# Kernel optimization log

Hardware: AMD Instinct MI355X
Metric: run time of the kernel (lower is better)

The kernel has to match this reference:

```python
import jax, jax.numpy as jnp
import numpy as np

B, S, D, H, E, K, F = 2, 512, 768, 12, 8, 2, 3072
HD = D // H
EPS = 1e-5


def setup_inputs() -> dict:
    key = jax.random.key(0)
    ks = jax.random.split(key, 8)
    sc = 0.02
    return {
        "x": jax.random.normal(ks[0], (B, S, D), jnp.float32),
        "ln1_w": jnp.ones((D,), jnp.float32),
        "ln1_b": jnp.zeros((D,), jnp.float32),
        "ln2_w": jnp.ones((D,), jnp.float32),
        "ln2_b": jnp.zeros((D,), jnp.float32),
        "w_qkv": jax.random.normal(ks[1], (D, 3 * D), jnp.float32) * sc,
        "b_qkv": jnp.zeros((3 * D,), jnp.float32),
        "w_out": jax.random.normal(ks[2], (D, D), jnp.float32) * sc,
        "b_out": jnp.zeros((D,), jnp.float32),
        "gate_w": jax.random.normal(ks[3], (D, E), jnp.float32) * sc,
        "w1": jax.random.normal(ks[4], (E, D, F), jnp.float32) * sc,
        "b1": jnp.zeros((E, F), jnp.float32),
        "w2": jax.random.normal(ks[5], (E, F, D), jnp.float32) * sc,
        "b2": jnp.zeros((E, D), jnp.float32),
    }


def _layernorm(x, w, b):
    mu = jnp.mean(x, axis=-1, keepdims=True)
    var = jnp.mean(jnp.square(x - mu), axis=-1, keepdims=True)
    return (x - mu) * jax.lax.rsqrt(var + EPS) * w + b


def _attention(x, w_qkv, b_qkv, w_out, b_out):
    qkv = x @ w_qkv + b_qkv                      # [B,S,3D]
    q, k, v = jnp.split(qkv, 3, axis=-1)
    q = q.reshape(B, S, H, HD)
    k = k.reshape(B, S, H, HD)
    v = v.reshape(B, S, H, HD)
    scores = jnp.einsum("bqhd,bkhd->bhqk", q, k) / jnp.sqrt(jnp.float32(HD))
    attn = jax.nn.softmax(scores, axis=-1)
    o = jnp.einsum("bhqk,bkhd->bqhd", attn, v).reshape(B, S, D)
    return o @ w_out + b_out


def _moe(x, gate_w, w1, b1, w2, b2):
    # x: [N, D] tokens. Top-k gating (fastmoe NaiveGate: softmax over top-k logits).
    logits = x @ gate_w                          # [N, E]
    topv, topi = jax.lax.top_k(logits, K)        # [N, K]
    gates = jax.nn.softmax(topv, axis=-1)        # [N, K]
    # combine weights as dense [N, E] (exact, no capacity drop)
    comb = jnp.sum(jax.nn.one_hot(topi, E, dtype=x.dtype) * gates[..., None], axis=1)
    h = jnp.einsum("nd,edf->enf", x, w1) + b1[:, None, :]   # [E, N, F]
    h = jax.nn.gelu(h)
    eo = jnp.einsum("enf,efd->end", h, w2) + b2[:, None, :]  # [E, N, D]
    return jnp.einsum("ne,end->nd", comb, eo)


def reference(x, ln1_w, ln1_b, ln2_w, ln2_b, w_qkv, b_qkv, w_out, b_out,
              gate_w, w1, b1, w2, b2):
    # Chunking over batch is a scheduling detail; whole-batch math is identical.
    h = _attention(_layernorm(x, ln1_w, ln1_b), w_qkv, b_qkv, w_out, b_out)
    x_resid = x + h
    moe_in = _layernorm(x_resid, ln2_w, ln2_b).reshape(B * S, D)
    moe_out = _moe(moe_in, gate_w, w1, b1, w2, b2).reshape(B, S, D)
    return moe_out + x_resid
```

## Files before the change

kernel.cpp:

```cpp
#include <hip/hip_runtime.h>
#include <hip/hip_bf16.h>

#define BB 2
#define SS 512
#define DD 768
#define HH 12
#define HDIM 64
#define EE 8
#define FF 3072
#define NTOK (BB*SS)
#define D3 (3*DD)
#define NSLOT (NTOK*2)

typedef unsigned short u16;
typedef unsigned int u32;
typedef __attribute__((ext_vector_type(8))) __bf16 bf16x8;
typedef __attribute__((ext_vector_type(4))) float f32x4;


__device__ __forceinline__ float gelu_tanh(float x) {
    float x3 = x * x * x;
    float z = 0.7978845608028654f * (x + 0.044715f * x3);
    float e = __expf(-2.f * z);
    float th = (1.f - e) / (1.f + e);
    return 0.5f * x * (1.f + th);
}

__device__ __forceinline__ u16 f2bf(float f) {
    union { float f; u32 u; } v; v.f = f;
    u32 r = v.u + 0x7FFF + ((v.u >> 16) & 1);
    return (u16)(r >> 16);
}

__device__ __forceinline__ float block_sum256(float v, float* red) {
    #pragma unroll
    for (int off = 32; off; off >>= 1) v += __shfl_down(v, off);
    int lane = threadIdx.x & 63, w = threadIdx.x >> 6;
    if (lane == 0) red[w] = v;
    __syncthreads();
    float tot = red[0] + red[1] + red[2] + red[3];
    __syncthreads();
    return tot;
}


__global__ __launch_bounds__(256) void k_ln(const float* __restrict__ x,
                                            const float* __restrict__ w,
                                            const float* __restrict__ b,
                                            float* __restrict__ out) {
    __shared__ float red[4];
    int t = blockIdx.x;
    const float* xr = x + (size_t)t * DD;
    int i = threadIdx.x;
    float v0 = xr[i], v1 = xr[i + 256], v2 = xr[i + 512];
    float mu = block_sum256(v0 + v1 + v2, red) * (1.f / 768.f);
    float d0 = v0 - mu, d1 = v1 - mu, d2 = v2 - mu;
    float var = block_sum256(d0 * d0 + d1 * d1 + d2 * d2, red) * (1.f / 768.f);
    float rs = rsqrtf(var + 1e-5f);
    float* o = out + (size_t)t * DD;
    o[i]       = d0 * rs * w[i]       + b[i];
    o[i + 256] = d1 * rs * w[i + 256] + b[i + 256];
    o[i + 512] = d2 * rs * w[i + 512] + b[i + 512];
}

__global__ __launch_bounds__(256) void k_ln_dual(const float* __restrict__ x,
                                                 const float* __restrict__ w,
                                                 const float* __restrict__ b,
                                                 float* __restrict__ out,
                                                 u16* __restrict__ outb) {
    __shared__ float red[4];
    int t = blockIdx.x;
    const float* xr = x + (size_t)t * DD;
    int i = threadIdx.x;
    float v0 = xr[i], v1 = xr[i + 256], v2 = xr[i + 512];
    float mu = block_sum256(v0 + v1 + v2, red) * (1.f / 768.f);
    float d0 = v0 - mu, d1 = v1 - mu, d2 = v2 - mu;
    float var = block_sum256(d0 * d0 + d1 * d1 + d2 * d2, red) * (1.f / 768.f);
    float rs = rsqrtf(var + 1e-5f);
    float* o = out + (size_t)t * DD;
    u16* ob = outb + (size_t)t * DD;
    float r0 = d0 * rs * w[i] + b[i];
    float r1 = d1 * rs * w[i + 256] + b[i + 256];
    float r2 = d2 * rs * w[i + 512] + b[i + 512];
    o[i] = r0; o[i + 256] = r1; o[i + 512] = r2;
    ob[i] = f2bf(r0); ob[i + 256] = f2bf(r1); ob[i + 512] = f2bf(r2);
}


template<int RES>
__global__ __launch_bounds__(256) void k_gemm(const float* __restrict__ A, int lda,
                                              const float* __restrict__ Bm, int ldb,
                                              const float* __restrict__ bias,
                                              const float* __restrict__ res,
                                              float* __restrict__ C, int ldc,
                                              int Kd) {
    __shared__ float As[16][68];
    __shared__ float Bs[16][64];
    int tid = threadIdx.x;
    int tx = tid & 15, ty = tid >> 4;
    int m0 = blockIdx.y * 64, n0 = blockIdx.x * 64;
    float acc[4][4] = {};
    for (int k0 = 0; k0 < Kd; k0 += 16) {
        #pragma unroll
        for (int i = 0; i < 4; ++i) {
            int idx = tid + i * 256;
            int mm = idx >> 4, kk = idx & 15;
            As[kk][mm] = A[(size_t)(m0 + mm) * lda + k0 + kk];
        }
        #pragma unroll
        for (int i = 0; i < 4; ++i) {
            int idx = tid + i * 256;
            int kk = idx >> 6, nn = idx & 63;
            Bs[kk][nn] = Bm[(size_t)(k0 + kk) * ldb + n0 + nn];
        }
        __syncthreads();
        #pragma unroll
        for (int kk = 0; kk < 16; ++kk) {
            float4 a4 = *reinterpret_cast<const float4*>(&As[kk][ty * 4]);
            float4 b4 = *reinterpret_cast<const float4*>(&Bs[kk][tx * 4]);
            float av[4] = {a4.x, a4.y, a4.z, a4.w};
            float bv[4] = {b4.x, b4.y, b4.z, b4.w};
            #pragma unroll
            for (int i = 0; i < 4; ++i)
                #pragma unroll
                for (int j = 0; j < 4; ++j) acc[i][j] += av[i] * bv[j];
        }
        __syncthreads();
    }
    #pragma unroll
    for (int i = 0; i < 4; ++i) {
        int row = m0 + ty * 4 + i;
        #pragma unroll
        for (int j = 0; j < 4; ++j) {
            int col = n0 + tx * 4 + j;
            float v = acc[i][j] + bias[col];
            if (RES) v += res[(size_t)row * ldc + col];
            C[(size_t)row * ldc + col] = v;
        }
    }
}


__global__ __launch_bounds__(256) void k_qk(const float* __restrict__ qkv,
                                            float* __restrict__ S) {
    int bh = blockIdx.z;
    int b = bh / HH, h = bh % HH;
    int m0 = blockIdx.y * 64, n0 = blockIdx.x * 64;
    const float* Q = qkv + (size_t)b * SS * D3 + h * HDIM;
    const float* Kp = Q + DD;
    __shared__ float As[16][68];
    __shared__ float Bs[16][68];
    int tid = threadIdx.x, tx = tid & 15, ty = tid >> 4;
    float acc[4][4] = {};
    for (int k0 = 0; k0 < HDIM; k0 += 16) {
        #pragma unroll
        for (int i = 0; i < 4; ++i) {
            int idx = tid + i * 256;
            int mm = idx >> 4, kk = idx & 15;
            As[kk][mm] = Q[(size_t)(m0 + mm) * D3 + k0 + kk];
            Bs[kk][mm] = Kp[(size_t)(n0 + mm) * D3 + k0 + kk];
        }
        __syncthreads();
        #pragma unroll
        for (int kk = 0; kk < 16; ++kk) {
            float4 a4 = *reinterpret_cast<const float4*>(&As[kk][ty * 4]);
            float4 b4 = *reinterpret_cast<const float4*>(&Bs[kk][tx * 4]);
            float av[4] = {a4.x, a4.y, a4.z, a4.w};
            float bv[4] = {b4.x, b4.y, b4.z, b4.w};
            #pragma unroll
            for (int i = 0; i < 4; ++i)
                #pragma unroll
                for (int j = 0; j < 4; ++j) acc[i][j] += av[i] * bv[j];
        }
        __syncthreads();
    }
    float* out = S + ((size_t)bh * SS + m0) * SS + n0;
    #pragma unroll
    for (int i = 0; i < 4; ++i)
        #pragma unroll
        for (int j = 0; j < 4; ++j)
            out[(size_t)(ty * 4 + i) * SS + tx * 4 + j] = acc[i][j] * 0.125f;
}

__global__ __launch_bounds__(64) void k_sm(float* __restrict__ S) {
    float* p = S + (size_t)blockIdx.x * SS;
    int lane = threadIdx.x;
    float v[8];
    float mx = -1e30f;
    #pragma unroll
    for (int j = 0; j < 8; ++j) { v[j] = p[lane + 64 * j]; mx = fmaxf(mx, v[j]); }
    #pragma unroll
    for (int off = 32; off; off >>= 1) mx = fmaxf(mx, __shfl_xor(mx, off));
    float s = 0.f;
    #pragma unroll
    for (int j = 0; j < 8; ++j) { v[j] = __expf(v[j] - mx); s += v[j]; }
    #pragma unroll
    for (int off = 32; off; off >>= 1) s += __shfl_xor(s, off);
    float inv = 1.f / s;
    #pragma unroll
    for (int j = 0; j < 8; ++j) p[lane + 64 * j] = v[j] * inv;
}

__global__ __launch_bounds__(256) void k_pv(const float* __restrict__ S,
                                            const float* __restrict__ qkv,
                                            float* __restrict__ attn_o) {
    int bh = blockIdx.y;
    int b = bh / HH, h = bh % HH;
    int m0 = blockIdx.x * 64;
    const float* P = S + (size_t)bh * SS * SS;
    const float* V = qkv + (size_t)b * SS * D3 + 2 * DD + h * HDIM;
    __shared__ float As[16][68];
    __shared__ float Bs[16][64];
    int tid = threadIdx.x, tx = tid & 15, ty = tid >> 4;
    float acc[4][4] = {};
    for (int k0 = 0; k0 < SS; k0 += 16) {
        #pragma unroll
        for (int i = 0; i < 4; ++i) {
            int idx = tid + i * 256;
            int mm = idx >> 4, kk = idx & 15;
            As[kk][mm] = P[(size_t)(m0 + mm) * SS + k0 + kk];
        }
        {
            int kk = tid >> 6, nn = tid & 63;
            #pragma unroll
            for (int i = 0; i < 4; ++i)
                Bs[kk + 4 * i][nn] = V[(size_t)(k0 + kk + 4 * i) * D3 + nn];
        }
        __syncthreads();
        #pragma unroll
        for (int kk = 0; kk < 16; ++kk) {
            float4 a4 = *reinterpret_cast<const float4*>(&As[kk][ty * 4]);
            float4 b4 = *reinterpret_cast<const float4*>(&Bs[kk][tx * 4]);
            float av[4] = {a4.x, a4.y, a4.z, a4.w};
            float bv[4] = {b4.x, b4.y, b4.z, b4.w};
            #pragma unroll
            for (int i = 0; i < 4; ++i)
                #pragma unroll
                for (int j = 0; j < 4; ++j) acc[i][j] += av[i] * bv[j];
        }
        __syncthreads();
    }
    float* O = attn_o + ((size_t)(b * SS + m0)) * DD + h * HDIM;
    #pragma unroll
    for (int i = 0; i < 4; ++i)
        #pragma unroll
        for (int j = 0; j < 4; ++j)
            O[(size_t)(ty * 4 + i) * DD + tx * 4 + j] = acc[i][j];
}


__global__ void k_zero(int* counts) {
    if (threadIdx.x < EE) counts[threadIdx.x] = 0;
}

__global__ __launch_bounds__(64) void k_gate(const float* __restrict__ X,
                                             const float* __restrict__ gw,
                                             int* __restrict__ gate_e,
                                             float* __restrict__ gate_v,
                                             int* __restrict__ gate_pos,
                                             int* __restrict__ counts) {
    int t = blockIdx.x;
    int lane = threadIdx.x;
    const float* xr = X + (size_t)t * DD;
    float acc[EE] = {};
    for (int d = lane; d < DD; d += 64) {
        float xv = xr[d];
        #pragma unroll
        for (int e = 0; e < EE; ++e) acc[e] += xv * gw[d * EE + e];
    }
    #pragma unroll
    for (int e = 0; e < EE; ++e)
        #pragma unroll
        for (int off = 32; off; off >>= 1) acc[e] += __shfl_xor(acc[e], off);
    if (lane == 0) {
        float v0 = -1e30f; int i0 = 0;
        #pragma unroll
        for (int e = 0; e < EE; ++e) if (acc[e] > v0) { v0 = acc[e]; i0 = e; }
        float v1 = -1e30f; int i1 = 0;
        #pragma unroll
        for (int e = 0; e < EE; ++e) if (e != i0 && acc[e] > v1) { v1 = acc[e]; i1 = e; }
        float e1v = expf(v1 - v0);
        float den = 1.f + e1v;
        int p0 = atomicAdd(&counts[i0], 1);
        int p1 = atomicAdd(&counts[i1], 1);
        gate_e[2 * t] = i0;        gate_e[2 * t + 1] = i1;
        gate_v[2 * t] = 1.f / den; gate_v[2 * t + 1] = e1v / den;
        gate_pos[2 * t] = p0;      gate_pos[2 * t + 1] = p1;
    }
}

__global__ void k_scan(const int* __restrict__ counts, int* __restrict__ base) {
    if (threadIdx.x == 0) {
        int s = 0;
        for (int e = 0; e < EE; ++e) { base[e] = s; s += counts[e]; }
    }
}

__global__ void k_fill(const int* __restrict__ gate_e, const int* __restrict__ gate_pos,
                       const int* __restrict__ base, int* __restrict__ slot_token) {
    int i = blockIdx.x * 256 + threadIdx.x;
    if (i < NSLOT) {
        int e = gate_e[i];
        slot_token[base[e] + gate_pos[i]] = i >> 1;
    }
}

__global__ __launch_bounds__(256) void k_cvtT(const float* __restrict__ src,
                                              u16* __restrict__ dst, int R, int C) {
    __shared__ float T[32][33];
    int e = blockIdx.z;
    const float* s = src + (size_t)e * R * C;
    u16* d = dst + (size_t)e * R * C;
    int c0 = blockIdx.x * 32, r0 = blockIdx.y * 32;
    int tx = threadIdx.x & 31, ty = threadIdx.x >> 5;
    #pragma unroll
    for (int i = 0; i < 4; ++i)
        T[ty + 8 * i][tx] = s[(size_t)(r0 + ty + 8 * i) * C + c0 + tx];
    __syncthreads();
    #pragma unroll
    for (int i = 0; i < 4; ++i)
        d[(size_t)(c0 + ty + 8 * i) * R + r0 + tx] = f2bf(T[tx][ty + 8 * i]);
}


__global__ __launch_bounds__(256) void k_moe1_mm(const u16* __restrict__ Xbf,
                                                 const u16* __restrict__ W1t,
                                                 const float* __restrict__ b1p,
                                                 const int* __restrict__ slot_token,
                                                 const int* __restrict__ base,
                                                 const int* __restrict__ counts,
                                                 u16* __restrict__ hbuf) {
    int e = blockIdx.z, cnt = counts[e];
    int mt = blockIdx.y;
    if (mt * 128 >= cnt) return;
    int bs = base[e];
    int n0 = blockIdx.x * 128;
    const u16* Bt = W1t + (size_t)e * DD * FF;
    __shared__ __align__(16) u16 As[128 * 32];
    __shared__ __align__(16) u16 Bs[128 * 32];
    __shared__ int Ms[128];
    int tid = threadIdx.x;
    if (tid < 128) {
        int r = mt * 128 + tid;
        Ms[tid] = slot_token[bs + ((r < cnt) ? r : 0)];
    }
    __syncthreads();
    int lane = tid & 63, wid = tid >> 6;
    int wm = wid >> 1, wn = wid & 1;
    f32x4 acc[4][4];
    #pragma unroll
    for (int i = 0; i < 4; ++i)
        #pragma unroll
        for (int j = 0; j < 4; ++j) acc[i][j] = (f32x4){0.f, 0.f, 0.f, 0.f};
    int arow = tid >> 2;
    int ac8 = (tid & 3) * 8;
    for (int k0 = 0; k0 < DD; k0 += 32) {
        uint4 a0 = *(const uint4*)(Xbf + (size_t)Ms[arow] * DD + k0 + ac8);
        uint4 a1 = *(const uint4*)(Xbf + (size_t)Ms[arow + 64] * DD + k0 + ac8);
        uint4 bq0 = *(const uint4*)(Bt + (size_t)(n0 + arow) * DD + k0 + ac8);
        uint4 bq1 = *(const uint4*)(Bt + (size_t)(n0 + arow + 64) * DD + k0 + ac8);
        __syncthreads();
        *(uint4*)(As + arow * 32 + ac8) = a0;
        *(uint4*)(As + (arow + 64) * 32 + ac8) = a1;
        *(uint4*)(Bs + arow * 32 + ac8) = bq0;
        *(uint4*)(Bs + (arow + 64) * 32 + ac8) = bq1;
        __syncthreads();
        bf16x8 af[4], bf[4];
        #pragma unroll
        for (int i = 0; i < 4; ++i) {
            af[i] = *(const bf16x8*)(As + (wm * 64 + i * 16 + (lane & 15)) * 32 + (lane >> 4) * 8);
            bf[i] = *(const bf16x8*)(Bs + (wn * 64 + i * 16 + (lane & 15)) * 32 + (lane >> 4) * 8);
        }
        #pragma unroll
        for (int mi = 0; mi < 4; ++mi)
            #pragma unroll
            for (int ni = 0; ni < 4; ++ni)
                acc[mi][ni] = __builtin_amdgcn_mfma_f32_16x16x32_bf16(af[mi], bf[ni], acc[mi][ni], 0, 0, 0);
    }
    #pragma unroll
    for (int mi = 0; mi < 4; ++mi) {
        int rb = mt * 128 + wm * 64 + mi * 16 + ((lane >> 4) << 2);
        #pragma unroll
        for (int ni = 0; ni < 4; ++ni) {
            int col = n0 + wn * 64 + ni * 16 + (lane & 15);
            float bv = b1p[e * FF + col];
            #pragma unroll
            for (int r = 0; r < 4; ++r) {
                int row = rb + r;
                if (row < cnt)
                    hbuf[(size_t)(bs + row) * FF + col] = f2bf(gelu_tanh(acc[mi][ni][r] + bv));
            }
        }
    }
}

__global__ __launch_bounds__(256) void k_moe2_mm(const u16* __restrict__ hbuf,
                                                 const u16* __restrict__ W2t,
                                                 const float* __restrict__ b2p,
                                                 const int* __restrict__ base,
                                                 const int* __restrict__ counts,
                                                 float* __restrict__ slot_out) {
    int e = blockIdx.z, cnt = counts[e];
    int mt = blockIdx.y;
    if (mt * 128 >= cnt) return;
    int bs = base[e];
    int n0 = blockIdx.x * 128;
    const u16* Bt = W2t + (size_t)e * DD * FF;
    __shared__ __align__(16) u16 As[128 * 32];
    __shared__ __align__(16) u16 Bs[128 * 32];
    int tid = threadIdx.x;
    int lane = tid & 63, wid = tid >> 6;
    int wm = wid >> 1, wn = wid & 1;
    f32x4 acc[4][4];
    #pragma unroll
    for (int i = 0; i < 4; ++i)
        #pragma unroll
        for (int j = 0; j < 4; ++j) acc[i][j] = (f32x4){0.f, 0.f, 0.f, 0.f};
    int arow = tid >> 2;
    int ac8 = (tid & 3) * 8;
    int r0g = mt * 128 + arow, r1g = r0g + 64;
    int rr0 = (r0g < cnt) ? r0g : 0;
    int rr1 = (r1g < cnt) ? r1g : 0;
    for (int k0 = 0; k0 < FF; k0 += 32) {
        uint4 a0 = *(const uint4*)(hbuf + (size_t)(bs + rr0) * FF + k0 + ac8);
        uint4 a1 = *(const uint4*)(hbuf + (size_t)(bs + rr1) * FF + k0 + ac8);
        uint4 bq0 = *(const uint4*)(Bt + (size_t)(n0 + arow) * FF + k0 + ac8);
        uint4 bq1 = *(const uint4*)(Bt + (size_t)(n0 + arow + 64) * FF + k0 + ac8);
        __syncthreads();
        *(uint4*)(As + arow * 32 + ac8) = a0;
        *(uint4*)(As + (arow + 64) * 32 + ac8) = a1;
        *(uint4*)(Bs + arow * 32 + ac8) = bq0;
        *(uint4*)(Bs + (arow + 64) * 32 + ac8) = bq1;
        __syncthreads();
        bf16x8 af[4], bf[4];
        #pragma unroll
        for (int i = 0; i < 4; ++i) {
            af[i] = *(const bf16x8*)(As + (wm * 64 + i * 16 + (lane & 15)) * 32 + (lane >> 4) * 8);
            bf[i] = *(const bf16x8*)(Bs + (wn * 64 + i * 16 + (lane & 15)) * 32 + (lane >> 4) * 8);
        }
        #pragma unroll
        for (int mi = 0; mi < 4; ++mi)
            #pragma unroll
            for (int ni = 0; ni < 4; ++ni)
                acc[mi][ni] = __builtin_amdgcn_mfma_f32_16x16x32_bf16(af[mi], bf[ni], acc[mi][ni], 0, 0, 0);
    }
    #pragma unroll
    for (int mi = 0; mi < 4; ++mi) {
        int rb = mt * 128 + wm * 64 + mi * 16 + ((lane >> 4) << 2);
        #pragma unroll
        for (int ni = 0; ni < 4; ++ni) {
            int col = n0 + wn * 64 + ni * 16 + (lane & 15);
            float bv = b2p[e * DD + col];
            #pragma unroll
            for (int r = 0; r < 4; ++r) {
                int row = rb + r;
                if (row < cnt)
                    slot_out[(size_t)(bs + row) * DD + col] = acc[mi][ni][r] + bv;
            }
        }
    }
}

__global__ __launch_bounds__(192) void k_combine(const float* __restrict__ xr,
                                                 const float* __restrict__ slot_out,
                                                 const int* __restrict__ gate_e,
                                                 const float* __restrict__ gate_v,
                                                 const int* __restrict__ gate_pos,
                                                 const int* __restrict__ base,
                                                 float* __restrict__ out) {
    int t = blockIdx.x;
    int e0 = gate_e[2 * t], e1 = gate_e[2 * t + 1];
    float g0 = gate_v[2 * t], g1 = gate_v[2 * t + 1];
    int s0 = base[e0] + gate_pos[2 * t];
    int s1 = base[e1] + gate_pos[2 * t + 1];
    int c = threadIdx.x * 4;
    float4 xv = *reinterpret_cast<const float4*>(xr + (size_t)t * DD + c);
    float4 a  = *reinterpret_cast<const float4*>(slot_out + (size_t)s0 * DD + c);
    float4 bq = *reinterpret_cast<const float4*>(slot_out + (size_t)s1 * DD + c);
    float4 r;
    r.x = xv.x + g0 * a.x + g1 * bq.x;
    r.y = xv.y + g0 * a.y + g1 * bq.y;
    r.z = xv.z + g0 * a.z + g1 * bq.z;
    r.w = xv.w + g0 * a.w + g1 * bq.w;
    *reinterpret_cast<float4*>(out + (size_t)t * DD + c) = r;
}


extern "C" void kernel_launch(void* const* d_in, const int* in_sizes, int n_in,
                              void* d_out, int out_size, void* d_ws, size_t ws_size,
                              hipStream_t stream) {
    const float* x      = (const float*)d_in[0];
    const float* ln1_w  = (const float*)d_in[1];
    const float* ln1_b  = (const float*)d_in[2];
    const float* ln2_w  = (const float*)d_in[3];
    const float* ln2_b  = (const float*)d_in[4];
    const float* w_qkv  = (const float*)d_in[5];
    const float* b_qkv  = (const float*)d_in[6];
    const float* w_out  = (const float*)d_in[7];
    const float* b_out  = (const float*)d_in[8];
    const float* gate_w = (const float*)d_in[9];
    const float* w1     = (const float*)d_in[10];
    const float* b1     = (const float*)d_in[11];
    const float* w2     = (const float*)d_in[12];
    const float* b2     = (const float*)d_in[13];
    float* out = (float*)d_out;

    char* p = (char*)d_ws;
    auto alloc = [&](size_t bytes) -> void* {
        void* r = (void*)p;
        p += (bytes + 255) & ~(size_t)255;
        return r;
    };
    float* ln1      = (float*)alloc((size_t)NTOK * DD * 4);
    float* qkvb     = (float*)alloc((size_t)NTOK * D3 * 4);
    float* attn_o   = (float*)alloc((size_t)NTOK * DD * 4);
    float* x_resid  = (float*)alloc((size_t)NTOK * DD * 4);
    float* moe_in   = (float*)alloc((size_t)NTOK * DD * 4);
    u16*   Xbf      = (u16*)alloc((size_t)NTOK * DD * 2);
    u16*   hbuf     = (u16*)alloc((size_t)NSLOT * FF * 2);
    float* slot_out = (float*)alloc((size_t)NSLOT * DD * 4);
    void*  region   = alloc((size_t)EE * DD * FF * 2);
    float* Smat = (float*)region;
    u16*   w1t  = (u16*)region;
    u16*   w2t  = (u16*)region;
    int*   gate_e   = (int*)alloc(NSLOT * 4);
    float* gate_v   = (float*)alloc(NSLOT * 4);
    int*   gate_pos = (int*)alloc(NSLOT * 4);
    int*   counts   = (int*)alloc(EE * 4);
    int*   base     = (int*)alloc(EE * 4);
    int*   slot_tok = (int*)alloc(NSLOT * 4);

    k_zero<<<1, 32, 0, stream>>>(counts);
    k_ln<<<NTOK, 256, 0, stream>>>(x, ln1_w, ln1_b, ln1);
    k_gemm<0><<<dim3(D3 / 64, NTOK / 64), 256, 0, stream>>>(
        ln1, DD, w_qkv, D3, b_qkv, nullptr, qkvb, D3, DD);
    k_qk<<<dim3(SS / 64, SS / 64, BB * HH), 256, 0, stream>>>(qkvb, Smat);
    k_sm<<<BB * HH * SS, 64, 0, stream>>>(Smat);
    k_pv<<<dim3(SS / 64, BB * HH), 256, 0, stream>>>(Smat, qkvb, attn_o);
    k_gemm<1><<<dim3(DD / 64, NTOK / 64), 256, 0, stream>>>(
        attn_o, DD, w_out, DD, b_out, x, x_resid, DD, DD);
    k_ln_dual<<<NTOK, 256, 0, stream>>>(x_resid, ln2_w, ln2_b, moe_in, Xbf);
    k_gate<<<NTOK, 64, 0, stream>>>(moe_in, gate_w, gate_e, gate_v, gate_pos, counts);
    k_scan<<<1, 1, 0, stream>>>(counts, base);
    k_fill<<<(NSLOT + 255) / 256, 256, 0, stream>>>(gate_e, gate_pos, base, slot_tok);
    k_cvtT<<<dim3(FF / 32, DD / 32, EE), 256, 0, stream>>>(w1, w1t, DD, FF);
    k_moe1_mm<<<dim3(FF / 128, NTOK / 128, EE), 256, 0, stream>>>(
        Xbf, w1t, b1, slot_tok, base, counts, hbuf);
    k_cvtT<<<dim3(DD / 32, FF / 32, EE), 256, 0, stream>>>(w2, w2t, FF, DD);
    k_moe2_mm<<<dim3(DD / 128, NTOK / 128, EE), 256, 0, stream>>>(
        hbuf, w2t, b2, base, counts, slot_out);
    k_combine<<<NTOK, 192, 0, stream>>>(x_resid, slot_out, gate_e, gate_v, gate_pos,
                                        base, out);
}
```

Baseline: 558.1 us.

## Move attention path to split-bf16 three-pass MFMA GEMMs

Replaces the fp32 scalar SIMT GEMMs for the QKV projection, QK^T, PV and output projection with bf16 MFMA kernels. Each operand is split into a hi and a lo bf16 part and multiplied in three passes (lo*hi, hi*lo, hi*hi) to keep roughly fp32 accuracy. New kernels convert and transpose the weights, Q, K and V into these split layouts, and softmax now writes split probabilities. This adds conversion passes and extra memory traffic for the split buffers, and runs three times the matrix-core work in exchange for much higher throughput than the scalar fp32 FMA loops.

```diff
diff --git a/kernel.cpp b/kernel.cpp
--- a/kernel.cpp
+++ b/kernel.cpp
@@ -11,6 +11,7 @@
 #define NTOK (BB*SS)
 #define D3 (3*DD)
 #define NSLOT (NTOK*2)
+#define NBH (BB*HH)
 
 typedef unsigned short u16;
 typedef unsigned int u32;
@@ -30,6 +31,11 @@
     union { float f; u32 u; } v; v.f = f;
     u32 r = v.u + 0x7FFF + ((v.u >> 16) & 1);
     return (u16)(r >> 16);
+}
+
+__device__ __forceinline__ float bf2f(u16 h) {
+    union { u32 u; float f; } v; v.u = ((u32)h) << 16;
+    return v.f;
 }
 
 __device__ __forceinline__ float block_sum256(float v, float* red) {
@@ -44,10 +50,11 @@
 }
 
 
-__global__ __launch_bounds__(256) void k_ln(const float* __restrict__ x,
-                                            const float* __restrict__ w,
-                                            const float* __restrict__ b,
-                                            float* __restrict__ out) {
+__global__ __launch_bounds__(256) void k_ln_split(const float* __restrict__ x,
+                                                  const float* __restrict__ w,
+                                                  const float* __restrict__ b,
+                                                  u16* __restrict__ oh,
+                                                  u16* __restrict__ ol) {
     __shared__ float red[4];
     int t = blockIdx.x;
     const float* xr = x + (size_t)t * DD;
@@ -57,10 +64,16 @@
     float d0 = v0 - mu, d1 = v1 - mu, d2 = v2 - mu;
     float var = block_sum256(d0 * d0 + d1 * d1 + d2 * d2, red) * (1.f / 768.f);
     float rs = rsqrtf(var + 1e-5f);
-    float* o = out + (size_t)t * DD;
-    o[i]       = d0 * rs * w[i]       + b[i];
-    o[i + 256] = d1 * rs * w[i + 256] + b[i + 256];
-    o[i + 512] = d2 * rs * w[i + 512] + b[i + 512];
+    u16* ph = oh + (size_t)t * DD;
+    u16* pl = ol + (size_t)t * DD;
+    float r0 = d0 * rs * w[i] + b[i];
+    float r1 = d1 * rs * w[i + 256] + b[i + 256];
+    float r2 = d2 * rs * w[i + 512] + b[i + 512];
+    u16 h0 = f2bf(r0), h1 = f2bf(r1), h2 = f2bf(r2);
+    ph[i] = h0; ph[i + 256] = h1; ph[i + 512] = h2;
+    pl[i] = f2bf(r0 - bf2f(h0));
+    pl[i + 256] = f2bf(r1 - bf2f(h1));
+    pl[i + 512] = f2bf(r2 - bf2f(h2));
 }
 
 __global__ __launch_bounds__(256) void k_ln_dual(const float* __restrict__ x,
@@ -86,104 +99,134 @@
     ob[i] = f2bf(r0); ob[i + 256] = f2bf(r1); ob[i + 512] = f2bf(r2);
 }
 
-
 template<int RES>
-__global__ __launch_bounds__(256) void k_gemm(const float* __restrict__ A, int lda,
-                                              const float* __restrict__ Bm, int ldb,
-                                              const float* __restrict__ bias,
-                                              const float* __restrict__ res,
-                                              float* __restrict__ C, int ldc,
-                                              int Kd) {
-    __shared__ float As[16][68];
-    __shared__ float Bs[16][64];
+__global__ __launch_bounds__(256) void k_gemm_x3b(const u16* __restrict__ Ah,
+                                                  const u16* __restrict__ Al,
+                                                  int lda, size_t sA,
+                                                  const u16* __restrict__ BtH,
+                                                  const u16* __restrict__ BtL,
+                                                  int ldb, size_t sB,
+                                                  const float* __restrict__ bias,
+                                                  const float* __restrict__ res,
+                                                  float* __restrict__ C,
+                                                  int ldc, size_t sC,
+                                                  int Kd, float scale) {
+    int z = blockIdx.z;
+    Ah += (size_t)z * sA; Al += (size_t)z * sA;
+    BtH += (size_t)z * sB; BtL += (size_t)z * sB;
+    C += (size_t)z * sC;
+    int m0 = blockIdx.y * 128, n0 = blockIdx.x * 128;
+    __shared__ __align__(16) u16 AsH[128 * 32];
+    __shared__ __align__(16) u16 AsL[128 * 32];
+    __shared__ __align__(16) u16 BsH[128 * 32];
+    __shared__ __align__(16) u16 BsL[128 * 32];
     int tid = threadIdx.x;
-    int tx = tid & 15, ty = tid >> 4;
-    int m0 = blockIdx.y * 64, n0 = blockIdx.x * 64;
-    float acc[4][4] = {};
-    for (int k0 = 0; k0 < Kd; k0 += 16) {
+    int lane = tid & 63, wid = tid >> 6;
+    int wm = wid >> 1, wn = wid & 1;
+    f32x4 acc[4][4];
+    #pragma unroll
+    for (int i = 0; i < 4; ++i)
+        #pragma unroll
+        for (int j = 0; j < 4; ++j) acc[i][j] = (f32x4){0.f, 0.f, 0.f, 0.f};
+    int arow = tid >> 2;
+    int ac8 = (tid & 3) * 8;
+    for (int k0 = 0; k0 < Kd; k0 += 32) {
+        uint4 a0h = *(const uint4*)(Ah + (size_t)(m0 + arow) * lda + k0 + ac8);
+        uint4 a1h = *(const uint4*)(Ah + (size_t)(m0 + arow + 64) * lda + k0 + ac8);
+        uint4 a0l = *(const uint4*)(Al + (size_t)(m0 + arow) * lda + k0 + ac8);
+        uint4 a1l = *(const uint4*)(Al + (size_t)(m0 + arow + 64) * lda + k0 + ac8);
+        uint4 b0h = *(const uint4*)(BtH + (size_t)(n0 + arow) * ldb + k0 + ac8);
+        uint4 b1h = *(const uint4*)(BtH + (size_t)(n0 + arow + 64) * ldb + k0 + ac8);
+        uint4 b0l = *(const uint4*)(BtL + (size_t)(n0 + arow) * ldb + k0 + ac8);
+        uint4 b1l = *(const uint4*)(BtL + (size_t)(n0 + arow + 64) * ldb + k0 + ac8);
+        __syncthreads();
+        *(uint4*)(AsH + arow * 32 + ac8) = a0h;
+        *(uint4*)(AsH + (arow + 64) * 32 + ac8) = a1h;
+        *(uint4*)(AsL + arow * 32 + ac8) = a0l;
+        *(uint4*)(AsL + (arow + 64) * 32 + ac8) = a1l;
+        *(uint4*)(BsH + arow * 32 + ac8) = b0h;
+        *(uint4*)(BsH + (arow + 64) * 32 + ac8) = b1h;
+        *(uint4*)(BsL + arow * 32 + ac8) = b0l;
+        *(uint4*)(BsL + (arow + 64) * 32 + ac8) = b1l;
+        __syncthreads();
+        bf16x8 afH[4], afL[4], bfH[4], bfL[4];
         #pragma unroll
         for (int i = 0; i < 4; ++i) {
-            int idx = tid + i * 256;
-            int mm = idx >> 4, kk = idx & 15;
-            As[kk][mm] = A[(size_t)(m0 + mm) * lda + k0 + kk];
-        }
-        #pragma unroll
-        for (int i = 0; i < 4; ++i) {
-            int idx = tid + i * 256;
-            int kk = idx >> 6, nn = idx & 63;
-            Bs[kk][nn] = Bm[(size_t)(k0 + kk) * ldb + n0 + nn];
-        }
-        __syncthreads();
-        #pragma unroll
-        for (int kk = 0; kk < 16; ++kk) {
-            float4 a4 = *reinterpret_cast<const float4*>(&As[kk][ty * 4]);
-            float4 b4 = *reinterpret_cast<const float4*>(&Bs[kk][tx * 4]);
-            float av[4] = {a4.x, a4.y, a4.z, a4.w};
-            float bv[4] = {b4.x, b4.y, b4.z, b4.w};
-            #pragma unroll
-            for (int i = 0; i < 4; ++i)
-                #pragma unroll
-                for (int j = 0; j < 4; ++j) acc[i][j] += av[i] * bv[j];
-        }
-        __syncthreads();
-    }
-    #pragma unroll
-    for (int i = 0; i < 4; ++i) {
-        int row = m0 + ty * 4 + i;
-        #pragma unroll
-        for (int j = 0; j < 4; ++j) {
-            int col = n0 + tx * 4 + j;
-            float v = acc[i][j] + bias[col];
-            if (RES) v += res[(size_t)row * ldc + col];
-            C[(size_t)row * ldc + col] = v;
-        }
-    }
-}
-
-
-__global__ __launch_bounds__(256) void k_qk(const float* __restrict__ qkv,
-                                            float* __restrict__ S) {
-    int bh = blockIdx.z;
+            int ao = (wm * 64 + i * 16 + (lane & 15)) * 32 + (lane >> 4) * 8;
+            int bo = (wn * 64 + i * 16 + (lane & 15)) * 32 + (lane >> 4) * 8;
+            afH[i] = *(const bf16x8*)(AsH + ao);
+            afL[i] = *(const bf16x8*)(AsL + ao);
+            bfH[i] = *(const bf16x8*)(BsH + bo);
+            bfL[i] = *(const bf16x8*)(BsL + bo);
+        }
+        #pragma unroll
+        for (int mi = 0; mi < 4; ++mi)
+            #pragma unroll
+            for (int ni = 0; ni < 4; ++ni) {
+                acc[mi][ni] = __builtin_amdgcn_mfma_f32_16x16x32_bf16(afL[mi], bfH[ni], acc[mi][ni], 0, 0, 0);
+                acc[mi][ni] = __builtin_amdgcn_mfma_f32_16x16x32_bf16(afH[mi], bfL[ni], acc[mi][ni], 0, 0, 0);
+                acc[mi][ni] = __builtin_amdgcn_mfma_f32_16x16x32_bf16(afH[mi], bfH[ni], acc[mi][ni], 0, 0, 0);
+            }
+    }
+    #pragma unroll
+    for (int mi = 0; mi < 4; ++mi) {
+        int rb = m0 + wm * 64 + mi * 16 + ((lane >> 4) << 2);
+        #pragma unroll
+        for (int ni = 0; ni < 4; ++ni) {
+            int col = n0 + wn * 64 + ni * 16 + (lane & 15);
+            float bv = bias ? bias[col] : 0.f;
+            #pragma unroll
+            for (int r = 0; r < 4; ++r) {
+                int row = rb + r;
+                float v = acc[mi][ni][r] * scale + bv;
+                if (RES) v += res[(size_t)row * ldc + col];
+                C[(size_t)row * ldc + col] = v;
+            }
+        }
+    }
+}
+
+
+__global__ __launch_bounds__(256) void k_attn_cvt(const float* __restrict__ qkvb,
+                                                  u16* __restrict__ qH, u16* __restrict__ qL,
+                                                  u16* __restrict__ kH, u16* __restrict__ kL,
+                                                  u16* __restrict__ vtH, u16* __restrict__ vtL) {
+    __shared__ float T[64][65];
+    int bh = blockIdx.y;
     int b = bh / HH, h = bh % HH;
-    int m0 = blockIdx.y * 64, n0 = blockIdx.x * 64;
-    const float* Q = qkv + (size_t)b * SS * D3 + h * HDIM;
-    const float* Kp = Q + DD;
-    __shared__ float As[16][68];
-    __shared__ float Bs[16][68];
-    int tid = threadIdx.x, tx = tid & 15, ty = tid >> 4;
-    float acc[4][4] = {};
-    for (int k0 = 0; k0 < HDIM; k0 += 16) {
-        #pragma unroll
-        for (int i = 0; i < 4; ++i) {
-            int idx = tid + i * 256;
-            int mm = idx >> 4, kk = idx & 15;
-            As[kk][mm] = Q[(size_t)(m0 + mm) * D3 + k0 + kk];
-            Bs[kk][mm] = Kp[(size_t)(n0 + mm) * D3 + k0 + kk];
-        }
-        __syncthreads();
-        #pragma unroll
-        for (int kk = 0; kk < 16; ++kk) {
-            float4 a4 = *reinterpret_cast<const float4*>(&As[kk][ty * 4]);
-            float4 b4 = *reinterpret_cast<const float4*>(&Bs[kk][tx * 4]);
-            float av[4] = {a4.x, a4.y, a4.z, a4.w};
-            float bv[4] = {b4.x, b4.y, b4.z, b4.w};
-            #pragma unroll
-            for (int i = 0; i < 4; ++i)
-                #pragma unroll
-                for (int j = 0; j < 4; ++j) acc[i][j] += av[i] * bv[j];
-        }
-        __syncthreads();
-    }
-    float* out = S + ((size_t)bh * SS + m0) * SS + n0;
-    #pragma unroll
-    for (int i = 0; i < 4; ++i)
-        #pragma unroll
-        for (int j = 0; j < 4; ++j)
-            out[(size_t)(ty * 4 + i) * SS + tx * 4 + j] = acc[i][j] * 0.125f;
-}
-
-__global__ __launch_bounds__(64) void k_sm(float* __restrict__ S) {
-    float* p = S + (size_t)blockIdx.x * SS;
+    int s0 = blockIdx.x * 64;
+    int tid = threadIdx.x;
+    #pragma unroll
+    for (int i = 0; i < 16; ++i) {
+        int idx = tid + i * 256;
+        int sl = idx >> 6, d = idx & 63;
+        size_t src = (size_t)(b * SS + s0 + sl) * D3 + h * HDIM + d;
+        float qv = qkvb[src];
+        float kv = qkvb[src + DD];
+        float vv = qkvb[src + 2 * DD];
+        size_t o = ((size_t)bh * SS + s0 + sl) * HDIM + d;
+        u16 qh = f2bf(qv); qH[o] = qh; qL[o] = f2bf(qv - bf2f(qh));
+        u16 kh = f2bf(kv); kH[o] = kh; kL[o] = f2bf(kv - bf2f(kh));
+        T[sl][d] = vv;
+    }
+    __syncthreads();
+    #pragma unroll
+    for (int i = 0; i < 16; ++i) {
+        int idx = tid + i * 256;
+        int dd = idx >> 6, sl = idx & 63;
+        float vv = T[sl][dd];
+        u16 vh = f2bf(vv);
+        size_t o = ((size_t)bh * HDIM + dd) * SS + s0 + sl;
+        vtH[o] = vh; vtL[o] = f2bf(vv - bf2f(vh));
+    }
+}
+
+__global__ __launch_bounds__(64) void k_sm_split(const float* __restrict__ S,
+                                                 u16* __restrict__ PHo,
+                                                 u16* __restrict__ PLo) {
+    const float* p = S + (size_t)blockIdx.x * SS;
+    u16* ph = PHo + (size_t)blockIdx.x * SS;
+    u16* pl = PLo + (size_t)blockIdx.x * SS;
     int lane = threadIdx.x;
     float v[8];
     float mx = -1e30f;
@@ -198,54 +241,93 @@
     for (int off = 32; off; off >>= 1) s += __shfl_xor(s, off);
     float inv = 1.f / s;
     #pragma unroll
-    for (int j = 0; j < 8; ++j) p[lane + 64 * j] = v[j] * inv;
-}
-
-__global__ __launch_bounds__(256) void k_pv(const float* __restrict__ S,
-                                            const float* __restrict__ qkv,
-                                            float* __restrict__ attn_o) {
+    for (int j = 0; j < 8; ++j) {
+        float w = v[j] * inv;
+        u16 hi = f2bf(w);
+        ph[lane + 64 * j] = hi;
+        pl[lane + 64 * j] = f2bf(w - bf2f(hi));
+    }
+}
+
+__global__ __launch_bounds__(256) void k_pv_x3(const u16* __restrict__ PHp,
+                                               const u16* __restrict__ PLp,
+                                               const u16* __restrict__ vtH,
+                                               const u16* __restrict__ vtL,
+                                               u16* __restrict__ oH,
+                                               u16* __restrict__ oL) {
     int bh = blockIdx.y;
     int b = bh / HH, h = bh % HH;
-    int m0 = blockIdx.x * 64;
-    const float* P = S + (size_t)bh * SS * SS;
-    const float* V = qkv + (size_t)b * SS * D3 + 2 * DD + h * HDIM;
-    __shared__ float As[16][68];
-    __shared__ float Bs[16][64];
-    int tid = threadIdx.x, tx = tid & 15, ty = tid >> 4;
-    float acc[4][4] = {};
-    for (int k0 = 0; k0 < SS; k0 += 16) {
+    int m0 = blockIdx.x * 128;
+    size_t abase = (size_t)bh * SS * SS;
+    size_t vbase = (size_t)bh * HDIM * SS;
+    __shared__ __align__(16) u16 AsH[128 * 32];
+    __shared__ __align__(16) u16 AsL[128 * 32];
+    __shared__ __align__(16) u16 BsH[64 * 32];
+    __shared__ __align__(16) u16 BsL[64 * 32];
+    int tid = threadIdx.x;
+    int lane = tid & 63, wid = tid >> 6;
+    int wm = wid >> 1, wn = wid & 1;
+    f32x4 acc[4][2];
+    #pragma unroll
+    for (int i = 0; i < 4; ++i)
+        #pragma unroll
+        for (int j = 0; j < 2; ++j) acc[i][j] = (f32x4){0.f, 0.f, 0.f, 0.f};
+    int arow = tid >> 2;
+    int ac8 = (tid & 3) * 8;
+    for (int k0 = 0; k0 < SS; k0 += 32) {
+        uint4 a0h = *(const uint4*)(PHp + abase + (size_t)(m0 + arow) * SS + k0 + ac8);
+        uint4 a1h = *(const uint4*)(PHp + abase + (size_t)(m0 + arow + 64) * SS + k0 + ac8);
+        uint4 a0l = *(const uint4*)(PLp + abase + (size_t)(m0 + arow) * SS + k0 + ac8);
+        uint4 a1l = *(const uint4*)(PLp + abase + (size_t)(m0 + arow + 64) * SS + k0 + ac8);
+        uint4 b0h = *(const uint4*)(vtH + vbase + (size_t)arow * SS + k0 + ac8);
+        uint4 b0l = *(const uint4*)(vtL + vbase + (size_t)arow * SS + k0 + ac8);
+        __syncthreads();
+        *(uint4*)(AsH + arow * 32 + ac8) = a0h;
+        *(uint4*)(AsH + (arow + 64) * 32 + ac8) = a1h;
+        *(uint4*)(AsL + arow * 32 + ac8) = a0l;
+        *(uint4*)(AsL + (arow + 64) * 32 + ac8) = a1l;
+        *(uint4*)(BsH + arow * 32 + ac8) = b0h;
+        *(uint4*)(BsL + arow * 32 + ac8) = b0l;
+        __syncthreads();
+        bf16x8 afH[4], afL[4], bfH[2], bfL[2];
         #pragma unroll
         for (int i = 0; i < 4; ++i) {
-            int idx = tid + i * 256;
-            int mm = idx >> 4, kk = idx & 15;
-            As[kk][mm] = P[(size_t)(m0 + mm) * SS + k0 + kk];
-        }
-        {
-            int kk = tid >> 6, nn = tid & 63;
-            #pragma unroll
-            for (int i = 0; i < 4; ++i)
-                Bs[kk + 4 * i][nn] = V[(size_t)(k0 + kk + 4 * i) * D3 + nn];
-        }
-        __syncthreads();
-        #pragma unroll
-        for (int kk = 0; kk < 16; ++kk) {
-            float4 a4 = *reinterpret_cast<const float4*>(&As[kk][ty * 4]);
-            float4 b4 = *reinterpret_cast<const float4*>(&Bs[kk][tx * 4]);
-            float av[4] = {a4.x, a4.y, a4.z, a4.w};
-            float bv[4] = {b4.x, b4.y, b4.z, b4.w};
-            #pragma unroll
-            for (int i = 0; i < 4; ++i)
-                #pragma unroll
-                for (int j = 0; j < 4; ++j) acc[i][j] += av[i] * bv[j];
-        }
-        __syncthreads();
-    }
-    float* O = attn_o + ((size_t)(b * SS + m0)) * DD + h * HDIM;
-    #pragma unroll
-    for (int i = 0; i < 4; ++i)
-        #pragma unroll
-        for (int j = 0; j < 4; ++j)
-            O[(size_t)(ty * 4 + i) * DD + tx * 4 + j] = acc[i][j];
+            int ao = (wm * 64 + i * 16 + (lane & 15)) * 32 + (lane >> 4) * 8;
+            afH[i] = *(const bf16x8*)(AsH + ao);
+            afL[i] = *(const bf16x8*)(AsL + ao);
+        }
+        #pragma unroll
+        for (int i = 0; i < 2; ++i) {
+            int bo = (wn * 32 + i * 16 + (lane & 15)) * 32 + (lane >> 4) * 8;
+            bfH[i] = *(const bf16x8*)(BsH + bo);
+            bfL[i] = *(const bf16x8*)(BsL + bo);
+        }
+        #pragma unroll
+        for (int mi = 0; mi < 4; ++mi)
+            #pragma unroll
+            for (int ni = 0; ni < 2; ++ni) {
+                acc[mi][ni] = __builtin_amdgcn_mfma_f32_16x16x32_bf16(afL[mi], bfH[ni], acc[mi][ni], 0, 0, 0);
+                acc[mi][ni] = __builtin_amdgcn_mfma_f32_16x16x32_bf16(afH[mi], bfL[ni], acc[mi][ni], 0, 0, 0);
+                acc[mi][ni] = __builtin_amdgcn_mfma_f32_16x16x32_bf16(afH[mi], bfH[ni], acc[mi][ni], 0, 0, 0);
+            }
+    }
+    #pragma unroll
+    for (int mi = 0; mi < 4; ++mi) {
+        int rb = m0 + wm * 64 + mi * 16 + ((lane >> 4) << 2);
+        #pragma unroll
+        for (int ni = 0; ni < 2; ++ni) {
+            int col = wn * 32 + ni * 16 + (lane & 15);
+            #pragma unroll
+            for (int r = 0; r < 4; ++r) {
+                int row = rb + r;
+                float v = acc[mi][ni][r];
+                u16 hi = f2bf(v);
+                size_t o = ((size_t)(b * SS + row)) * DD + h * HDIM + col;
+                oH[o] = hi;
+                oL[o] = f2bf(v - bf2f(hi));
+            }
+        }
+    }
 }
 
 
@@ -305,6 +387,7 @@
     }
 }
 
+
 __global__ __launch_bounds__(256) void k_cvtT(const float* __restrict__ src,
                                               u16* __restrict__ dst, int R, int C) {
     __shared__ float T[32][33];
@@ -320,6 +403,28 @@
     #pragma unroll
     for (int i = 0; i < 4; ++i)
         d[(size_t)(c0 + ty + 8 * i) * R + r0 + tx] = f2bf(T[tx][ty + 8 * i]);
+}
+
+__global__ __launch_bounds__(256) void k_cvtT_split(const float* __restrict__ src,
+                                                    u16* __restrict__ dstH,
+                                                    u16* __restrict__ dstL,
+                                                    int R, int C) {
+    __shared__ float T[32][33];
+    const float* s = src;
+    int c0 = blockIdx.x * 32, r0 = blockIdx.y * 32;
+    int tx = threadIdx.x & 31, ty = threadIdx.x >> 5;
+    #pragma unroll
+    for (int i = 0; i < 4; ++i)
+        T[ty + 8 * i][tx] = s[(size_t)(r0 + ty + 8 * i) * C + c0 + tx];
+    __syncthreads();
+    #pragma unroll
+    for (int i = 0; i < 4; ++i) {
+        float v = T[tx][ty + 8 * i];
+        u16 hi = f2bf(v);
+        size_t idx = (size_t)(c0 + ty + 8 * i) * R + r0 + tx;
+        dstH[idx] = hi;
+        dstL[idx] = f2bf(v - bf2f(hi));
+    }
 }
 
 
@@ -511,16 +616,32 @@
         p += (bytes + 255) & ~(size_t)255;
         return r;
     };
-    float* ln1      = (float*)alloc((size_t)NTOK * DD * 4);
+    u16*   ln1H     = (u16*)alloc((size_t)NTOK * DD * 2);
+    u16*   ln1L     = (u16*)alloc((size_t)NTOK * DD * 2);
     float* qkvb     = (float*)alloc((size_t)NTOK * D3 * 4);
-    float* attn_o   = (float*)alloc((size_t)NTOK * DD * 4);
+    u16*   qHb      = (u16*)alloc((size_t)NBH * SS * HDIM * 2);
+    u16*   qLb      = (u16*)alloc((size_t)NBH * SS * HDIM * 2);
+    u16*   kHb      = (u16*)alloc((size_t)NBH * SS * HDIM * 2);
+    u16*   kLb      = (u16*)alloc((size_t)NBH * SS * HDIM * 2);
+    u16*   vtHb     = (u16*)alloc((size_t)NBH * SS * HDIM * 2);
+    u16*   vtLb     = (u16*)alloc((size_t)NBH * SS * HDIM * 2);
+    u16*   attn_oH  = (u16*)alloc((size_t)NTOK * DD * 2);
+    u16*   attn_oL  = (u16*)alloc((size_t)NTOK * DD * 2);
     float* x_resid  = (float*)alloc((size_t)NTOK * DD * 4);
     float* moe_in   = (float*)alloc((size_t)NTOK * DD * 4);
     u16*   Xbf      = (u16*)alloc((size_t)NTOK * DD * 2);
     u16*   hbuf     = (u16*)alloc((size_t)NSLOT * FF * 2);
     float* slot_out = (float*)alloc((size_t)NSLOT * DD * 4);
-    void*  region   = alloc((size_t)EE * DD * FF * 2);
+    u16*   wqkvtH   = (u16*)alloc((size_t)D3 * DD * 2);
+    u16*   wqkvtL   = (u16*)alloc((size_t)D3 * DD * 2);
+    u16*   wouttH   = (u16*)alloc((size_t)DD * DD * 2);
+    u16*   wouttL   = (u16*)alloc((size_t)DD * DD * 2);
+    const size_t S_BYTES  = (size_t)NBH * SS * SS * 4;
+    const size_t PH_BYTES = (size_t)NBH * SS * SS * 2;
+    char* region = (char*)alloc(S_BYTES + 2 * PH_BYTES);
     float* Smat = (float*)region;
+    u16*   PHb  = (u16*)(region + S_BYTES);
+    u16*   PLb  = (u16*)(region + S_BYTES + PH_BYTES);
     u16*   w1t  = (u16*)region;
     u16*   w2t  = (u16*)region;
     int*   gate_e   = (int*)alloc(NSLOT * 4);
@@ -531,14 +652,19 @@
     int*   slot_tok = (int*)alloc(NSLOT * 4);
 
     k_zero<<<1, 32, 0, stream>>>(counts);
-    k_ln<<<NTOK, 256, 0, stream>>>(x, ln1_w, ln1_b, ln1);
-    k_gemm<0><<<dim3(D3 / 64, NTOK / 64), 256, 0, stream>>>(
-        ln1, DD, w_qkv, D3, b_qkv, nullptr, qkvb, D3, DD);
-    k_qk<<<dim3(SS / 64, SS / 64, BB * HH), 256, 0, stream>>>(qkvb, Smat);
-    k_sm<<<BB * HH * SS, 64, 0, stream>>>(Smat);
-    k_pv<<<dim3(SS / 64, BB * HH), 256, 0, stream>>>(Smat, qkvb, attn_o);
-    k_gemm<1><<<dim3(DD / 64, NTOK / 64), 256, 0, stream>>>(
-        attn_o, DD, w_out, DD, b_out, x, x_resid, DD, DD);
+    k_ln_split<<<NTOK, 256, 0, stream>>>(x, ln1_w, ln1_b, ln1H, ln1L);
+    k_cvtT_split<<<dim3(D3 / 32, DD / 32), 256, 0, stream>>>(w_qkv, wqkvtH, wqkvtL, DD, D3);
+    k_gemm_x3b<0><<<dim3(D3 / 128, NTOK / 128, 1), 256, 0, stream>>>(
+        ln1H, ln1L, DD, 0, wqkvtH, wqkvtL, DD, 0, b_qkv, nullptr, qkvb, D3, 0, DD, 1.f);
+    k_attn_cvt<<<dim3(SS / 64, NBH), 256, 0, stream>>>(qkvb, qHb, qLb, kHb, kLb, vtHb, vtLb);
+    k_gemm_x3b<0><<<dim3(SS / 128, SS / 128, NBH), 256, 0, stream>>>(
+        qHb, qLb, HDIM, (size_t)SS * HDIM, kHb, kLb, HDIM, (size_t)SS * HDIM,
+        nullptr, nullptr, Smat, SS, (size_t)SS * SS, HDIM, 0.125f);
+    k_sm_split<<<NBH * SS, 64, 0, stream>>>(Smat, PHb, PLb);
+    k_pv_x3<<<dim3(SS / 128, NBH), 256, 0, stream>>>(PHb, PLb, vtHb, vtLb, attn_oH, attn_oL);
+    k_cvtT_split<<<dim3(DD / 32, DD / 32), 256, 0, stream>>>(w_out, wouttH, wouttL, DD, DD);
+    k_gemm_x3b<1><<<dim3(DD / 128, NTOK / 128, 1), 256, 0, stream>>>(
+        attn_oH, attn_oL, DD, 0, wouttH, wouttL, DD, 0, b_out, x, x_resid, DD, 0, DD, 1.f);
     k_ln_dual<<<NTOK, 256, 0, stream>>>(x_resid, ln2_w, ln2_b, moe_in, Xbf);
     k_gate<<<NTOK, 64, 0, stream>>>(moe_in, gate_w, gate_e, gate_v, gate_pos, counts);
     k_scan<<<1, 1, 0, stream>>>(counts, base);
```

Result: faster. 477.5 us (-14.5%).
